# Performance work log

Hardware: AMD Instinct MI355X
Metric: run time of the kernel (lower is better)

## Reference

```python
import jax, jax.numpy as jnp
import numpy as np

NBINS = (128, 64, 32)
LOG2PI = float(np.log(2.0 * np.pi))


def _quadratic_spline_stack(x, genes_oi, local_gene_ix, delta, uh, uw):
    """Stack of piecewise-quadratic (piecewise-linear density) splines on [0,1].
    Per split with n heights / n-1 widths (n-1 bins). Returns (outputs, logabsdet)."""
    uh_oi = uh[genes_oi]  # [G, sum(n)]
    uw_oi = uw[genes_oi]  # [G, sum(n-1)]
    outputs = x
    logabsdet = jnp.zeros_like(x)
    oh = ow = od = 0
    for n in NBINS:
        nh, nw = n, n - 1
        uhs = uh_oi[:, oh:oh + nh]
        uws = uw_oi[:, ow:ow + nw]
        ds = delta[:, od:od + nh]
        oh += nh; ow += nw; od += nh
        # per-gene bin widths / locations
        widths_g = jax.nn.softmax(uws, axis=-1)                     # [G, nw]
        bl = jnp.cumsum(widths_g, axis=-1)
        bl = bl.at[:, -1].set(1.0)
        bin_loc_g = jnp.pad(bl, ((0, 0), (1, 0)))                   # [G, nw+1]
        # gather per cut
        w = widths_g[local_gene_ix]                                 # [N, nw]
        loc = bin_loc_g[local_gene_ix]                              # [N, nw+1]
        # per-cut knot heights: gene baseline + cell/gene delta, normalized to unit area
        h_un = jnp.exp(uhs[local_gene_ix] + ds)                     # [N, nh]
        area = jnp.sum(0.5 * (h_un[:, :-1] + h_un[:, 1:]) * w, axis=-1, keepdims=True)
        h = h_un / area                                             # [N, nh]
        seg = 0.5 * (h[:, :-1] + h[:, 1:]) * w                      # bin masses [N, nw]
        left_cdf = jnp.pad(jnp.cumsum(seg, axis=-1)[:, :-1], ((0, 0), (1, 0)))  # [N, nw]
        # locate bin
        bin_idx = jnp.clip(jnp.sum(outputs[:, None] >= loc, axis=-1) - 1, 0, nw - 1)
        gi = bin_idx[:, None]
        loc_l = jnp.take_along_axis(loc, gi, -1)[:, 0]
        w_b = jnp.take_along_axis(w, gi, -1)[:, 0]
        cdf_l = jnp.take_along_axis(left_cdf, gi, -1)[:, 0]
        h_l = jnp.take_along_axis(h, gi, -1)[:, 0]
        h_r = jnp.take_along_axis(h, gi + 1, -1)[:, 0]
        alpha = (outputs - loc_l) / w_b
        outputs = (0.5 * (h_r - h_l) * w_b) * alpha * alpha + h_l * w_b * alpha + cdf_l
        logabsdet = logabsdet + jnp.log(h_l + (h_r - h_l) * alpha)
    return outputs, logabsdet


def setup_inputs() -> dict:
    key = jax.random.key(0)
    ks = jax.random.split(key, 10)
    B, L, G_total, G_oi, C, N = 512, 16, 20000, 500, 224, 200000
    clustering = jax.random.uniform(ks[0], (B, L), dtype=jnp.float32)
    coordinates = jax.random.uniform(ks[1], (N,), dtype=jnp.float32, minval=1e-4, maxval=1.0 - 1e-4)
    genes_oi = jax.random.randint(ks[2], (G_oi,), 0, G_total)
    local_gene_ix = jax.random.randint(ks[3], (N,), 0, G_oi)
    local_cellxgene_ix = jax.random.randint(ks[4], (N,), 0, B * G_oi)
    localcellxgene_ix = jax.random.randint(ks[5], (N,), 0, B * G_total)
    logit_weight = jax.random.normal(ks[6], (G_total, L, C), dtype=jnp.float32) * 0.01
    rho_weight = jax.random.normal(ks[7], (G_total, L), dtype=jnp.float32) * 0.05
    rho_bias = 1e-5 + (1.0 - 1e-5) * jax.random.uniform(ks[8], (G_total,), dtype=jnp.float32)
    k9, k10 = jax.random.split(ks[9])
    unnormalized_heights = jax.random.normal(k9, (G_total, sum(NBINS)), dtype=jnp.float32) * 0.1
    unnormalized_widths = jax.random.normal(k10, (G_total, sum(n - 1 for n in NBINS)), dtype=jnp.float32) * 0.1
    return dict(clustering=clustering, coordinates=coordinates, genes_oi=genes_oi,
                local_gene_ix=local_gene_ix, local_cellxgene_ix=local_cellxgene_ix,
                localcellxgene_ix=localcellxgene_ix, logit_weight=logit_weight,
                rho_weight=rho_weight, rho_bias=rho_bias,
                unnormalized_heights=unnormalized_heights,
                unnormalized_widths=unnormalized_widths)


def reference(clustering, coordinates, genes_oi, local_gene_ix, local_cellxgene_ix,
              localcellxgene_ix, logit_weight, rho_weight, rho_bias,
              unnormalized_heights, unnormalized_widths):
    B = clustering.shape[0]
    G = genes_oi.shape[0]
    n_total_genes = rho_bias.shape[0]
    # Decoder (n_layers=0 -> nn_output = latent)
    lw_oi = logit_weight[genes_oi]                                   # [G, L, C]
    mixture_delta = jnp.einsum('bl,glc->bgc', clustering, lw_oi)     # [B, G, C]
    rho_delta = clustering @ rho_weight.T                            # [B, G_total]
    rho = jax.nn.softmax(jnp.log(rho_bias)[None, :] + rho_delta, axis=-1)
    rho_cuts = rho.reshape(-1)[localcellxgene_ix]                    # [N]
    md_cuts = mixture_delta.reshape(B * G, -1)[local_cellxgene_ix]   # [N, C]
    _, lik_mixture = _quadratic_spline_stack(coordinates, genes_oi, local_gene_ix,
                                             md_cuts, unnormalized_heights, unnormalized_widths)
    lik_overall = jnp.log(rho_cuts) + jnp.log(jnp.float32(n_total_genes))
    elbo = -jnp.sum(lik_mixture + lik_overall)
    # Normal(0, exp(log_scale=0)=1) regularization log-probs
    def normal_logpdf(v):
        return -0.5 * v * v - 0.5 * LOG2PI
    elbo = elbo - jnp.sum(normal_logpdf(lw_oi))
    elbo = elbo - jnp.sum(normal_logpdf(rho_weight[genes_oi]))
    return elbo
```

## Files before the change

### kernel.cpp

```cpp
#include <hip/hip_runtime.h>
#include <cstddef>

#define LOG2PI_F 1.8378770664093453f

__device__ __forceinline__ float wave_sum(float v) {
#pragma unroll
    for (int o = 32; o >= 1; o >>= 1) v += __shfl_xor(v, o, 64);
    return v;
}
__device__ __forceinline__ float wave_max(float v) {
#pragma unroll
    for (int o = 32; o >= 1; o >>= 1) v = fmaxf(v, __shfl_xor(v, o, 64));
    return v;
}
__device__ __forceinline__ float wave_scan_incl(float v, int lane) {
#pragma unroll
    for (int o = 1; o < 64; o <<= 1) {
        float t = __shfl_up(v, o, 64);
        if (lane >= o) v += t;
    }
    return v;
}

__global__ void k_logrb(const float* __restrict__ rho_bias, float* __restrict__ logrb, int G_total) {
    int g = blockIdx.x * blockDim.x + threadIdx.x;
    if (g < G_total) logrb[g] = __logf(rho_bias[g]);
}

__global__ void k_prep_genes(const int* __restrict__ genes_oi,
                             const float* __restrict__ uh, const float* __restrict__ uw,
                             float4* __restrict__ pk) {
    const int g = blockIdx.x;
    const int t = threadIdx.x;
    const int gs = genes_oi[g];
    const float* uhg = uh + (size_t)gs * 224;
    const float* uwg = uw + (size_t)gs * 221;
    float4* pkg = pk + (size_t)g * 224;

    const int NH[3] = {128, 64, 32};
    const int OH[3] = {0, 128, 192};
    const int OW[3] = {0, 127, 190};
    const int SO[3] = {0, 128, 191};
#pragma unroll
    for (int lev = 0; lev < 3; ++lev) {
        const int nw = NH[lev] - 1;
        float v0 = (t < nw)      ? uwg[OW[lev] + t]      : -INFINITY;
        float v1 = (t + 64 < nw) ? uwg[OW[lev] + t + 64] : -INFINITY;
        float mx = wave_max(fmaxf(v0, v1));
        float e0 = (t < nw)      ? __expf(v0 - mx) : 0.f;
        float e1 = (t + 64 < nw) ? __expf(v1 - mx) : 0.f;
        float inv = 1.0f / wave_sum(e0 + e1);
        float w0 = e0 * inv, w1 = e1 * inv;
        float i0 = wave_scan_incl(w0, t);
        float tot0 = __shfl(i0, 63, 64);
        float i1 = wave_scan_incl(w1, t) + tot0;
        if (t < nw) {
            float loc = (t == nw - 1) ? 1.0f : i0;
            pkg[SO[lev] + t] = make_float4(uhg[OH[lev] + t + 1], 0.5f * w0, loc, 0.f);
        }
        if (t + 64 < nw) {
            int j = t + 64;
            float loc = (j == nw - 1) ? 1.0f : i1;
            pkg[SO[lev] + j] = make_float4(uhg[OH[lev] + j + 1], 0.5f * w1, loc, 0.f);
        }
    }
    if (t == 0) pkg[127] = make_float4(uhg[0], uhg[128], uhg[192], 0.f);
}

__global__ void k_prep_lwT(const int* __restrict__ genes_oi,
                           const float* __restrict__ lw, const float* __restrict__ rw,
                           float* __restrict__ lwT, float* __restrict__ pB) {
    const int g = blockIdx.x;
    const int tid = threadIdx.x;
    const int gs = genes_oi[g];
    const float* src = lw + (size_t)gs * 3584;
    float* dst = lwT + (size_t)g * 3584;
    float acc = 0.f;
    if (tid < 224) {
        float vv[16];
#pragma unroll
        for (int l = 0; l < 16; ++l) {
            float v = src[l * 224 + tid];
            vv[l] = v;
            acc = fmaf(v, v, acc);
        }
        float4* d4 = (float4*)(dst + (size_t)tid * 16);
#pragma unroll
        for (int q = 0; q < 4; ++q)
            d4[q] = make_float4(vv[4 * q + 0], vv[4 * q + 1], vv[4 * q + 2], vv[4 * q + 3]);
    }
    if (tid < 16) { float v = rw[(size_t)gs * 16 + tid]; acc = fmaf(v, v, acc); }
    __shared__ float sm[256];
    sm[tid] = acc;
    __syncthreads();
    for (int o = 128; o > 0; o >>= 1) { if (tid < o) sm[tid] += sm[tid + o]; __syncthreads(); }
    if (tid == 0) pB[g] = 0.5f * sm[0] + 0.5f * LOG2PI_F * (3584.0f + 16.0f);
}

__global__ void k_lse(const float* __restrict__ clustering, const float* __restrict__ rw,
                      const float* __restrict__ logrb, float* __restrict__ lse, int G_total) {
    const int b = blockIdx.x;
    const int tid = threadIdx.x;
    __shared__ float cl_s[16];
    if (tid < 16) cl_s[tid] = clustering[(size_t)b * 16 + tid];
    __syncthreads();
    float m = -INFINITY, s = 0.f;
    for (int g = tid; g < G_total; g += blockDim.x) {
        const float4* r4 = (const float4*)(rw + (size_t)g * 16);
        float d = 0.f;
#pragma unroll
        for (int q = 0; q < 4; ++q) {
            float4 v = r4[q];
            d = fmaf(cl_s[4 * q + 0], v.x, d);
            d = fmaf(cl_s[4 * q + 1], v.y, d);
            d = fmaf(cl_s[4 * q + 2], v.z, d);
            d = fmaf(cl_s[4 * q + 3], v.w, d);
        }
        float logit = logrb[g] + d;
        float mn = fmaxf(m, logit);
        s = s * __expf(m - mn) + __expf(logit - mn);
        m = mn;
    }
    __shared__ float ms[256], ss[256];
    ms[tid] = m; ss[tid] = s;
    __syncthreads();
    for (int o = 128; o > 0; o >>= 1) {
        if (tid < o) {
            float m2 = ms[tid + o], s2 = ss[tid + o];
            float mn = fmaxf(ms[tid], m2);
            ss[tid] = ss[tid] * __expf(ms[tid] - mn) + s2 * __expf(m2 - mn);
            ms[tid] = mn;
        }
        __syncthreads();
    }
    if (tid == 0) lse[b] = ms[0] + __logf(ss[0]);
}

__global__ void k_zero(int* __restrict__ p, int n) {
    int i = blockIdx.x * blockDim.x + threadIdx.x;
    if (i < n) p[i] = 0;
}

__global__ void k_hist(const int* __restrict__ lcx, int* __restrict__ counts, int N, int G_oi) {
    int i = blockIdx.x * blockDim.x + threadIdx.x;
    if (i < N) atomicAdd(&counts[(unsigned)lcx[i] % (unsigned)G_oi], 1);
}

__global__ void k_scan(const int* __restrict__ counts, int* __restrict__ offsets,
                       int* __restrict__ cursor, int G_oi) {
    __shared__ int sm[512];
    const int t = threadIdx.x;
    int v = (t < G_oi) ? counts[t] : 0;
    sm[t] = v;
    __syncthreads();
    for (int o = 1; o < 512; o <<= 1) {
        int add = (t >= o) ? sm[t - o] : 0;
        __syncthreads();
        sm[t] += add;
        __syncthreads();
    }
    if (t < G_oi) {
        offsets[t + 1] = sm[t];
        cursor[t] = sm[t] - v;
    }
    if (t == 0) offsets[0] = 0;
}

__global__ void k_scatter(const float* __restrict__ coord, const int* __restrict__ lgix,
                          const int* __restrict__ lcx, const int* __restrict__ lc2,
                          int* __restrict__ cursor,
                          float* __restrict__ xs, int* __restrict__ b1s,
                          int* __restrict__ lc2s, int* __restrict__ ghs, int N, int G_oi) {
    int i = blockIdx.x * blockDim.x + threadIdx.x;
    if (i >= N) return;
    unsigned v = (unsigned)lcx[i];
    unsigned g = v % (unsigned)G_oi;
    int pos = atomicAdd(&cursor[g], 1);
    xs[pos]   = coord[i];
    b1s[pos]  = (int)(v / (unsigned)G_oi);
    lc2s[pos] = lc2[i];
    ghs[pos]  = lgix[i];
}

__launch_bounds__(512, 4)
__global__ void k_main2(const float* __restrict__ xs, const int* __restrict__ b1s,
                        const int* __restrict__ lc2s, const int* __restrict__ ghs,
                        const int* __restrict__ offsets,
                        const float* __restrict__ clustering,
                        const float* __restrict__ lwT,
                        const float4* __restrict__ pk,
                        const float* __restrict__ rw,
                        const float* __restrict__ logrb,
                        const float* __restrict__ lse,
                        float* __restrict__ pA, int G_oi, int G_total) {
    const int g = blockIdx.x;
    const int tid = threadIdx.x;
    const float* lwg = lwT + (size_t)g * 3584;
    const int s = offsets[g], e = offsets[g + 1];
    const float logGt = __logf((float)G_total);
    float acc = 0.f;

    for (int base = s; base < e; base += 512) {
        const int i = base + tid;
        const bool valid = i < e;
        const int isafe = valid ? i : s;
        float x = xs[isafe];
        const int b1  = b1s[isafe];
        const int lc2 = lc2s[isafe];
        const int gh  = ghs[isafe];
        const float4* pkh = pk + (size_t)gh * 224;

        float cl[16];
        {
            const float4* c4 = (const float4*)(clustering + (size_t)b1 * 16);
#pragma unroll
            for (int q = 0; q < 4; ++q) {
                float4 v = c4[q];
                cl[4 * q + 0] = v.x; cl[4 * q + 1] = v.y; cl[4 * q + 2] = v.z; cl[4 * q + 3] = v.w;
            }
        }
        const float4 uh0 = pkh[127];
        const float uh0v[3] = {uh0.x, uh0.y, uh0.z};

        float lad = 0.f;
        const int NH[3] = {128, 64, 32};
        const int OH[3] = {0, 128, 192};
        const int SO[3] = {0, 128, 191};
#pragma unroll
        for (int lev = 0; lev < 3; ++lev) {
            const int nw = NH[lev] - 1;
            const float* rowbase = lwg + (size_t)OH[lev] * 16;
            float hp;
            {
                float d = 0.f;
#pragma unroll
                for (int l = 0; l < 16; ++l) d = fmaf(cl[l], rowbase[l], d);
                hp = __expf(uh0v[lev] + d);
            }
            float h_l = hp, h_r = hp, whb = 0.f, loc_l = 0.f, cdf = 0.f, area = 0.f;
            int in = 0;
            const float4* pks = pkh + SO[lev];
            for (int j = 0; j < nw; ++j) {
                const float* row = rowbase + (size_t)(j + 1) * 16;
                float d = 0.f;
#pragma unroll
                for (int l = 0; l < 16; ++l) d = fmaf(cl[l], row[l], d);
                float4 pkv = pks[j];
                float hn = __expf(pkv.x + d);
                float seg = (hp + hn) * pkv.y;
                bool inJ = (in == j);
                if (inJ) { h_r = hn; whb = pkv.y; }
                bool adv = (x >= pkv.z) && (j < nw - 1);
                if (adv) { cdf += seg; h_l = hn; loc_l = pkv.z; in = j + 1; }
                area += seg;
                hp = hn;
            }
            float inv_area = __builtin_amdgcn_rcpf(area);
            float alpha = (x - loc_l) * 0.5f * __builtin_amdgcn_rcpf(whb);
            float t2 = whb * alpha;
            x = (t2 * fmaf(h_r - h_l, alpha, 2.f * h_l) + cdf) * inv_area;
            lad += __logf(fmaf(h_r - h_l, alpha, h_l)) - __logf(area);
        }

        unsigned b2 = (unsigned)lc2 / (unsigned)G_total;
        unsigned gt = (unsigned)lc2 - b2 * (unsigned)G_total;
        float d2 = 0.f;
        {
            const float4* c24 = (const float4*)(clustering + (size_t)b2 * 16);
            const float4* r4  = (const float4*)(rw + (size_t)gt * 16);
#pragma unroll
            for (int q = 0; q < 4; ++q) {
                float4 a = c24[q], b = r4[q];
                d2 = fmaf(a.x, b.x, d2); d2 = fmaf(a.y, b.y, d2);
                d2 = fmaf(a.z, b.z, d2); d2 = fmaf(a.w, b.w, d2);
            }
        }
        float lik = logrb[gt] + d2 - lse[b2] + logGt;
        if (valid) acc -= (lad + lik);
    }

    acc = wave_sum(acc);
    __shared__ float wsm[8];
    if ((tid & 63) == 0) wsm[tid >> 6] = acc;
    __syncthreads();
    if (tid == 0) {
        float t = 0.f;
#pragma unroll
        for (int w = 0; w < 8; ++w) t += wsm[w];
        pA[g] = t;
    }
}

__global__ void k_final(const float* __restrict__ pA, const float* __restrict__ pB,
                        float* __restrict__ out, int nA, int nB) {
    const int tid = threadIdx.x;
    float acc = 0.f;
    for (int i = tid; i < nA; i += blockDim.x) acc += pA[i];
    for (int i = tid; i < nB; i += blockDim.x) acc += pB[i];
    __shared__ float sm[256];
    sm[tid] = acc;
    __syncthreads();
    for (int o = 128; o > 0; o >>= 1) { if (tid < o) sm[tid] += sm[tid + o]; __syncthreads(); }
    if (tid == 0) out[0] = sm[0];
}

extern "C" void kernel_launch(void* const* d_in, const int* in_sizes, int n_in,
                              void* d_out, int out_size, void* d_ws, size_t ws_size,
                              hipStream_t stream) {
    const float* clustering        = (const float*)d_in[0];
    const float* coordinates       = (const float*)d_in[1];
    const int*   genes_oi          = (const int*)d_in[2];
    const int*   local_gene_ix     = (const int*)d_in[3];
    const int*   local_cellxgene_ix= (const int*)d_in[4];
    const int*   localcellxgene_ix = (const int*)d_in[5];
    const float* lw                = (const float*)d_in[6];
    const float* rw                = (const float*)d_in[7];
    const float* rho_bias          = (const float*)d_in[8];
    const float* uh                = (const float*)d_in[9];
    const float* uw                = (const float*)d_in[10];

    const int G_total = in_sizes[8];
    const int G_oi    = in_sizes[2];
    const int N       = in_sizes[1];
    const int L       = in_sizes[7] / G_total;
    const int B       = in_sizes[0] / L;

    size_t off = 0;
    char* base = (char*)d_ws;
    auto alloc = [&](size_t nbytes) {
        char* p = base + off;
        off = (off + nbytes + 15) & ~(size_t)15;
        return (void*)p;
    };
    float*  pA      = (float*)alloc(sizeof(float) * (G_oi + 16));
    float*  pB      = (float*)alloc(sizeof(float) * (G_oi + 16));
    float*  lse     = (float*)alloc(sizeof(float) * (B + 16));
    float*  logrb   = (float*)alloc(sizeof(float) * G_total);
    float*  lwT     = (float*)alloc(sizeof(float) * (size_t)G_oi * 3584);
    float4* pk      = (float4*)alloc(sizeof(float4) * (size_t)G_oi * 224);
    int*    counts  = (int*)alloc(sizeof(int) * 512);
    int*    offsets = (int*)alloc(sizeof(int) * 512);
    int*    cursor  = (int*)alloc(sizeof(int) * 512);
    float*  xs      = (float*)alloc(sizeof(float) * N);
    int*    b1s     = (int*)alloc(sizeof(int) * N);
    int*    lc2s    = (int*)alloc(sizeof(int) * N);
    int*    ghs     = (int*)alloc(sizeof(int) * N);
    (void)ws_size;

    const int TPB = 256;
    k_logrb<<<(G_total + TPB - 1) / TPB, TPB, 0, stream>>>(rho_bias, logrb, G_total);
    k_prep_genes<<<G_oi, 64, 0, stream>>>(genes_oi, uh, uw, pk);
    k_prep_lwT<<<G_oi, 256, 0, stream>>>(genes_oi, lw, rw, lwT, pB);
    k_lse<<<B, 256, 0, stream>>>(clustering, rw, logrb, lse, G_total);
    k_zero<<<2, 256, 0, stream>>>(counts, 512);
    k_hist<<<(N + TPB - 1) / TPB, TPB, 0, stream>>>(local_cellxgene_ix, counts, N, G_oi);
    k_scan<<<1, 512, 0, stream>>>(counts, offsets, cursor, G_oi);
    k_scatter<<<(N + TPB - 1) / TPB, TPB, 0, stream>>>(coordinates, local_gene_ix,
                                                       local_cellxgene_ix, localcellxgene_ix,
                                                       cursor, xs, b1s, lc2s, ghs, N, G_oi);
    k_main2<<<G_oi, 512, 0, stream>>>(xs, b1s, lc2s, ghs, offsets, clustering, lwT, pk,
                                      rw, logrb, lse, pA, G_oi, G_total);
    k_final<<<1, 256, 0, stream>>>(pA, pB, (float*)d_out, G_oi, G_oi);
}
```

Before: 672.2 us.

## Interleave spline params by gene, sort cuts by gene in-block, batch LSE rows

Measured after the change: 647.6 us. 3.6% less time.

```diff
diff --git a/kernel.cpp b/kernel.cpp
--- a/kernel.cpp
+++ b/kernel.cpp
@@ -29,13 +29,12 @@
 
 __global__ void k_prep_genes(const int* __restrict__ genes_oi,
                              const float* __restrict__ uh, const float* __restrict__ uw,
-                             float4* __restrict__ pk) {
+                             float4* __restrict__ pk, int G_oi) {
     const int g = blockIdx.x;
     const int t = threadIdx.x;
     const int gs = genes_oi[g];
     const float* uhg = uh + (size_t)gs * 224;
     const float* uwg = uw + (size_t)gs * 221;
-    float4* pkg = pk + (size_t)g * 224;
 
     const int NH[3] = {128, 64, 32};
     const int OH[3] = {0, 128, 192};
@@ -56,15 +55,15 @@
         float i1 = wave_scan_incl(w1, t) + tot0;
         if (t < nw) {
             float loc = (t == nw - 1) ? 1.0f : i0;
-            pkg[SO[lev] + t] = make_float4(uhg[OH[lev] + t + 1], 0.5f * w0, loc, 0.f);
+            pk[(size_t)(SO[lev] + t) * G_oi + g] = make_float4(uhg[OH[lev] + t + 1], 0.5f * w0, loc, 0.f);
         }
         if (t + 64 < nw) {
             int j = t + 64;
             float loc = (j == nw - 1) ? 1.0f : i1;
-            pkg[SO[lev] + j] = make_float4(uhg[OH[lev] + j + 1], 0.5f * w1, loc, 0.f);
-        }
-    }
-    if (t == 0) pkg[127] = make_float4(uhg[0], uhg[128], uhg[192], 0.f);
+            pk[(size_t)(SO[lev] + j) * G_oi + g] = make_float4(uhg[OH[lev] + j + 1], 0.5f * w1, loc, 0.f);
+        }
+    }
+    if (t == 0) pk[(size_t)127 * G_oi + g] = make_float4(uhg[0], uhg[128], uhg[192], 0.f);
 }
 
 __global__ void k_prep_lwT(const int* __restrict__ genes_oi,
@@ -97,43 +96,74 @@
     if (tid == 0) pB[g] = 0.5f * sm[0] + 0.5f * LOG2PI_F * (3584.0f + 16.0f);
 }
 
-__global__ void k_lse(const float* __restrict__ clustering, const float* __restrict__ rw,
-                      const float* __restrict__ logrb, float* __restrict__ lse, int G_total) {
-    const int b = blockIdx.x;
+__global__ void k_lse4(const float* __restrict__ clustering, const float* __restrict__ rw,
+                       const float* __restrict__ logrb, float* __restrict__ lse,
+                       int G_total, int B) {
+    const int b0 = blockIdx.x * 4;
     const int tid = threadIdx.x;
-    __shared__ float cl_s[16];
-    if (tid < 16) cl_s[tid] = clustering[(size_t)b * 16 + tid];
-    __syncthreads();
-    float m = -INFINITY, s = 0.f;
-    for (int g = tid; g < G_total; g += blockDim.x) {
+    const int nc = min(4, B - b0);
+
+    float cl[4][16];
+#pragma unroll
+    for (int c = 0; c < 4; ++c) {
+        if (c < nc) {
+            const float4* c4 = (const float4*)(clustering + (size_t)(b0 + c) * 16);
+#pragma unroll
+            for (int q = 0; q < 4; ++q) {
+                float4 v = c4[q];
+                cl[c][4 * q + 0] = v.x; cl[c][4 * q + 1] = v.y;
+                cl[c][4 * q + 2] = v.z; cl[c][4 * q + 3] = v.w;
+            }
+        } else {
+#pragma unroll
+            for (int l = 0; l < 16; ++l) cl[c][l] = 0.f;
+        }
+    }
+
+    float m[4], s[4];
+#pragma unroll
+    for (int c = 0; c < 4; ++c) { m[c] = -INFINITY; s[c] = 0.f; }
+
+    for (int g = tid; g < G_total; g += 256) {
         const float4* r4 = (const float4*)(rw + (size_t)g * 16);
-        float d = 0.f;
-#pragma unroll
-        for (int q = 0; q < 4; ++q) {
-            float4 v = r4[q];
-            d = fmaf(cl_s[4 * q + 0], v.x, d);
-            d = fmaf(cl_s[4 * q + 1], v.y, d);
-            d = fmaf(cl_s[4 * q + 2], v.z, d);
-            d = fmaf(cl_s[4 * q + 3], v.w, d);
-        }
-        float logit = logrb[g] + d;
-        float mn = fmaxf(m, logit);
-        s = s * __expf(m - mn) + __expf(logit - mn);
-        m = mn;
-    }
-    __shared__ float ms[256], ss[256];
-    ms[tid] = m; ss[tid] = s;
+        float4 rv[4];
+#pragma unroll
+        for (int q = 0; q < 4; ++q) rv[q] = r4[q];
+        const float lb = logrb[g];
+#pragma unroll
+        for (int c = 0; c < 4; ++c) {
+            float d = 0.f;
+#pragma unroll
+            for (int q = 0; q < 4; ++q) {
+                d = fmaf(cl[c][4 * q + 0], rv[q].x, d);
+                d = fmaf(cl[c][4 * q + 1], rv[q].y, d);
+                d = fmaf(cl[c][4 * q + 2], rv[q].z, d);
+                d = fmaf(cl[c][4 * q + 3], rv[q].w, d);
+            }
+            float logit = lb + d;
+            float mn = fmaxf(m[c], logit);
+            s[c] = s[c] * __expf(m[c] - mn) + __expf(logit - mn);
+            m[c] = mn;
+        }
+    }
+
+    __shared__ float ms[4][256], ss[4][256];
+#pragma unroll
+    for (int c = 0; c < 4; ++c) { ms[c][tid] = m[c]; ss[c][tid] = s[c]; }
     __syncthreads();
     for (int o = 128; o > 0; o >>= 1) {
         if (tid < o) {
-            float m2 = ms[tid + o], s2 = ss[tid + o];
-            float mn = fmaxf(ms[tid], m2);
-            ss[tid] = ss[tid] * __expf(ms[tid] - mn) + s2 * __expf(m2 - mn);
-            ms[tid] = mn;
-        }
-        __syncthreads();
-    }
-    if (tid == 0) lse[b] = ms[0] + __logf(ss[0]);
+#pragma unroll
+            for (int c = 0; c < 4; ++c) {
+                float m2 = ms[c][tid + o], s2 = ss[c][tid + o];
+                float mn = fmaxf(ms[c][tid], m2);
+                ss[c][tid] = ss[c][tid] * __expf(ms[c][tid] - mn) + s2 * __expf(m2 - mn);
+                ms[c][tid] = mn;
+            }
+        }
+        __syncthreads();
+    }
+    if (tid < 4 && tid < nc) lse[b0 + tid] = ms[tid][0] + __logf(ss[tid][0]);
 }
 
 __global__ void k_zero(int* __restrict__ p, int n) {
@@ -200,26 +230,58 @@
     const float logGt = __logf((float)G_total);
     float acc = 0.f;
 
+    __shared__ int   s_cnt[512];
+    __shared__ int   s_cur[512];
+    __shared__ float s_x[512];
+    __shared__ int2  s_meta[512];
+    __shared__ float wsm[8];
+
     for (int base = s; base < e; base += 512) {
+        const int cnt = min(512, e - base);
         const int i = base + tid;
-        const bool valid = i < e;
+        const bool valid = tid < cnt;
         const int isafe = valid ? i : s;
-        float x = xs[isafe];
-        const int b1  = b1s[isafe];
-        const int lc2 = lc2s[isafe];
-        const int gh  = ghs[isafe];
-        const float4* pkh = pk + (size_t)gh * 224;
+        float x0   = xs[isafe];
+        int   b1_0 = b1s[isafe];
+        int   lc2_0= lc2s[isafe];
+        int   gh_0 = ghs[isafe];
+
+        s_cnt[tid] = 0;
+        __syncthreads();
+        if (valid) atomicAdd(&s_cnt[gh_0], 1);
+        __syncthreads();
+        int v = s_cnt[tid];
+        for (int o = 1; o < 512; o <<= 1) {
+            int add = (tid >= o) ? s_cnt[tid - o] : 0;
+            __syncthreads();
+            s_cnt[tid] += add;
+            __syncthreads();
+        }
+        s_cur[tid] = s_cnt[tid] - v;
+        __syncthreads();
+        if (valid) {
+            int pos = atomicAdd(&s_cur[gh_0], 1);
+            s_x[pos]    = x0;
+            s_meta[pos] = make_int2((b1_0 << 16) | gh_0, lc2_0);
+        }
+        __syncthreads();
+        const int rd = valid ? tid : 0;
+        float x  = s_x[rd];
+        int2 mt  = s_meta[rd];
+        const int gh  = mt.x & 0xffff;
+        const int b1  = mt.x >> 16;
+        const int lc2 = mt.y;
 
         float cl[16];
         {
             const float4* c4 = (const float4*)(clustering + (size_t)b1 * 16);
 #pragma unroll
             for (int q = 0; q < 4; ++q) {
-                float4 v = c4[q];
-                cl[4 * q + 0] = v.x; cl[4 * q + 1] = v.y; cl[4 * q + 2] = v.z; cl[4 * q + 3] = v.w;
-            }
-        }
-        const float4 uh0 = pkh[127];
+                float4 vv = c4[q];
+                cl[4 * q + 0] = vv.x; cl[4 * q + 1] = vv.y; cl[4 * q + 2] = vv.z; cl[4 * q + 3] = vv.w;
+            }
+        }
+        const float4 uh0 = pk[(size_t)127 * G_oi + gh];
         const float uh0v[3] = {uh0.x, uh0.y, uh0.z};
 
         float lad = 0.f;
@@ -239,13 +301,14 @@
             }
             float h_l = hp, h_r = hp, whb = 0.f, loc_l = 0.f, cdf = 0.f, area = 0.f;
             int in = 0;
-            const float4* pks = pkh + SO[lev];
+            const float4* pks = pk + (size_t)SO[lev] * G_oi + gh;
             for (int j = 0; j < nw; ++j) {
                 const float* row = rowbase + (size_t)(j + 1) * 16;
                 float d = 0.f;
 #pragma unroll
                 for (int l = 0; l < 16; ++l) d = fmaf(cl[l], row[l], d);
-                float4 pkv = pks[j];
+                float4 pkv = *pks;
+                pks += G_oi;
                 float hn = __expf(pkv.x + d);
                 float seg = (hp + hn) * pkv.y;
                 bool inJ = (in == j);
@@ -280,7 +343,6 @@
     }
 
     acc = wave_sum(acc);
-    __shared__ float wsm[8];
     if ((tid & 63) == 0) wsm[tid >> 6] = acc;
     __syncthreads();
     if (tid == 0) {
@@ -349,9 +411,9 @@
 
     const int TPB = 256;
     k_logrb<<<(G_total + TPB - 1) / TPB, TPB, 0, stream>>>(rho_bias, logrb, G_total);
-    k_prep_genes<<<G_oi, 64, 0, stream>>>(genes_oi, uh, uw, pk);
+    k_prep_genes<<<G_oi, 64, 0, stream>>>(genes_oi, uh, uw, pk, G_oi);
     k_prep_lwT<<<G_oi, 256, 0, stream>>>(genes_oi, lw, rw, lwT, pB);
-    k_lse<<<B, 256, 0, stream>>>(clustering, rw, logrb, lse, G_total);
+    k_lse4<<<(B + 3) / 4, 256, 0, stream>>>(clustering, rw, logrb, lse, G_total, B);
     k_zero<<<2, 256, 0, stream>>>(counts, 512);
     k_hist<<<(N + TPB - 1) / TPB, TPB, 0, stream>>>(local_cellxgene_ix, counts, N, G_oi);
     k_scan<<<1, 512, 0, stream>>>(counts, offsets, cursor, G_oi);
```
